# Optimization experiments

Measured on AMD Instinct MI355X. Metric: run time of the kernel, lower is better.

## Reference

```python
import jax, jax.numpy as jnp
import numpy as np

B, D, C = 4096, 2048, 64
L_HP, D_HP, OMEGA, EPSILON = 0.5, 1.0, 100.0, 0.1
LN_EPS = 1e-5
CLASS_COUNTS = [5000,4500,4050,3645,3280,2952,2657,2391,2152,1937,1743,1569,1412,1271,1144,1029,926,834,750,675,608,547,492,443,399,359,323,291,262,236,212,191,172,155,139,125,113,101,91,82,74,66,60,54,48,43,39,35,32,28,26,23,21,19,17,15,14,12,11,10,9,8,7,7]


def setup_inputs() -> dict:
    key = jax.random.key(0)
    k_x, k_y, k_b, k_u1, k_u2 = jax.random.split(key, 5)
    counts = jnp.asarray(CLASS_COUNTS, dtype=jnp.float32)
    # set_class_weights: tilde_C = 1/log(counts*d + eps), min-max normalized, scaled by l
    tilde = 1.0 / jnp.log(counts * D_HP + EPSILON)
    c = (tilde - jnp.min(tilde)) / (jnp.max(tilde) - jnp.min(tilde)) * L_HP
    # set_fs_classes: 1 where count <= omega
    fs_classes = jnp.where(counts <= OMEGA, 1, 0).astype(jnp.int32)
    x = jax.random.normal(k_x, (B, D), dtype=jnp.float32)
    y = jax.random.randint(k_y, (B,), 0, C)
    beta_idx = jax.random.randint(k_b, (B,), 0, B)
    u1 = jax.random.uniform(k_u1, (B,))
    u2 = jax.random.uniform(k_u2, (B,))
    alpha = jnp.where(u1 > 0.5, u2, jnp.ones((B,), jnp.float32))
    return {"x": x, "y": y, "alpha": alpha, "beta_idx": beta_idx, "c": c, "fs_classes": fs_classes}


def reference(x, y, alpha, beta_idx, c, fs_classes):
    n_batch, dim = x.shape
    num_classes = c.shape[0]
    # --- reconstruct ---
    mu = jnp.mean(x, axis=-1, keepdims=True)
    var = jnp.mean((x - mu) ** 2, axis=-1, keepdims=True)
    x_norm = (x - mu) / jnp.sqrt(var + LN_EPS) / jnp.sqrt(jnp.asarray(dim, x.dtype))
    sim = jnp.matmul(x_norm, x_norm.T)  # [B, B]
    # E[i, j] = eye[i, j] + fs_mask[j]  (broadcast over rows), thresholded to {0, 1}
    fs_mask = fs_classes[y].astype(x.dtype)  # [B]
    E = jnp.eye(n_batch, dtype=x.dtype) + fs_mask[None, :]
    E = jnp.where(E >= 1.0, 1.0, 0.0)
    sim = jax.nn.softmax(sim - 100000.0 * E, axis=-1)
    contrib = c[y]  # [B]
    reconstructions = jnp.matmul(sim, x)  # [B, D]
    R = reconstructions * contrib[:, None] + x * (1.0 - contrib)[:, None]
    # --- pairwise_mix: M @ R with M[i,:] = alpha[i]*e_i + (1-alpha[i])*e_{beta_idx[i]} ---
    y_oh = jax.nn.one_hot(y, num_classes, dtype=x.dtype)
    a = alpha[:, None]
    x_mix = a * R + (1.0 - a) * R[beta_idx]
    y_mix = a * y_oh + (1.0 - a) * y_oh[beta_idx]
    return (x_mix, y_mix)
```

## Files before the change

### kernel.cpp

```cpp
#include <hip/hip_runtime.h>
#include <cstdint>
#include <cstddef>

typedef __bf16 bf16;
typedef __bf16 bf16x8 __attribute__((ext_vector_type(8)));
typedef float floatx4 __attribute__((ext_vector_type(4)));
typedef int intx8 __attribute__((ext_vector_type(8)));

#define NB 4096
#define ND 2048
#define NCLS 64
#define TS 80
#define OS 72

__device__ __forceinline__ void stage16(const void* g, void* l) {
  __builtin_amdgcn_global_load_lds(
      (__attribute__((address_space(1))) unsigned int*)g,
      (__attribute__((address_space(3))) unsigned int*)l, 16, 0, 0);
}

__device__ __forceinline__ unsigned char fp8x1(float f) {
  return (unsigned char)(__builtin_amdgcn_cvt_pk_fp8_f32(f, f, 0, false) & 0xFF);
}
__device__ __forceinline__ int fp8x4(float f0, float f1, float f2, float f3) {
  int d = __builtin_amdgcn_cvt_pk_fp8_f32(f0, f1, 0, false);
  return __builtin_amdgcn_cvt_pk_fp8_f32(f2, f3, d, true);
}

__device__ __forceinline__ void gemm_core64(
    const unsigned char* __restrict__ Abase, const int aoff[4],
    const unsigned char* __restrict__ Bbase, const int boff[2], int nk,
    unsigned char* __restrict__ As0, unsigned char* __restrict__ Bs0,
    unsigned char* __restrict__ As1, unsigned char* __restrict__ Bs1,
    floatx4 acc[2][4], int w, int lane) {
  const int lm = lane & 15, quad = lane >> 4;
  auto STAGE = [&](int k0, unsigned char* As, unsigned char* Bs) {
#pragma unroll
    for (int q = 0; q < 4; ++q)
      stage16(Abase + (size_t)(aoff[q] + k0), As + w * 4096 + q * 1024);
#pragma unroll
    for (int q = 0; q < 2; ++q)
      stage16(Bbase + (size_t)(boff[q] + k0), Bs + w * 2048 + q * 1024);
  };
  STAGE(0, As0, Bs0);
  for (int k = 0; k < nk; ++k) {
    __syncthreads();
    if (k + 1 < nk)
      STAGE((k + 1) << 7, (k & 1) ? As0 : As1, (k & 1) ? Bs0 : Bs1);
    const unsigned char* Ac = (k & 1) ? As1 : As0;
    const unsigned char* Bc = (k & 1) ? Bs1 : Bs0;

    intx8 af[2], bf[4];
#pragma unroll
    for (int i = 0; i < 2; ++i) {
      const int row = w * 32 + i * 16 + lm;
      const int c0 = (quad * 2) ^ (row & 7);
      const int4 lo = *(const int4*)(Ac + row * 128 + c0 * 16);
      const int4 hi = *(const int4*)(Ac + row * 128 + (c0 ^ 1) * 16);
      af[i][0] = lo.x; af[i][1] = lo.y; af[i][2] = lo.z; af[i][3] = lo.w;
      af[i][4] = hi.x; af[i][5] = hi.y; af[i][6] = hi.z; af[i][7] = hi.w;
    }
#pragma unroll
    for (int i = 0; i < 4; ++i) {
      const int row = i * 16 + lm;
      const int c0 = (quad * 2) ^ (row & 7);
      const int4 lo = *(const int4*)(Bc + row * 128 + c0 * 16);
      const int4 hi = *(const int4*)(Bc + row * 128 + (c0 ^ 1) * 16);
      bf[i][0] = lo.x; bf[i][1] = lo.y; bf[i][2] = lo.z; bf[i][3] = lo.w;
      bf[i][4] = hi.x; bf[i][5] = hi.y; bf[i][6] = hi.z; bf[i][7] = hi.w;
    }
#pragma unroll
    for (int mi = 0; mi < 2; ++mi)
#pragma unroll
      for (int ni = 0; ni < 4; ++ni)
        acc[mi][ni] = __builtin_amdgcn_mfma_scale_f32_16x16x128_f8f6f4(
            af[mi], bf[ni], acc[mi][ni], 0, 0, 0, 127, 0, 127);
  }
}


__global__ __launch_bounds__(1024) void perm_kernel(
    const int* __restrict__ y, const int* __restrict__ fs,
    const float* __restrict__ c, int* __restrict__ perm,
    int* __restrict__ minfo, float* __restrict__ lrow,
    float* __restrict__ contrib) {
  const int t = threadIdx.x;
  const int base = t * 4;
  int fl[4];
  int cnt = 0;
#pragma unroll
  for (int j = 0; j < 4; ++j) {
    const int yi = y[base + j];
    fl[j] = (fs[yi] == 0) ? 1 : 0;
    cnt += fl[j];
    contrib[base + j] = c[yi];
    lrow[base + j] = 0.0f;
  }
  const int lane = t & 63, w = t >> 6;
  int inc = cnt;
#pragma unroll
  for (int o = 1; o < 64; o <<= 1) {
    int v = __shfl_up(inc, o);
    if (lane >= o) inc += v;
  }
  __shared__ int wsum[16];
  __shared__ int Msh;
  if (lane == 63) wsum[w] = inc;
  __syncthreads();
  int wbase = 0;
  for (int i = 0; i < w; ++i) wbase += wsum[i];
  int pos = wbase + inc - cnt;
#pragma unroll
  for (int j = 0; j < 4; ++j)
    if (fl[j]) perm[pos++] = base + j;
  if (t == 1023) Msh = wbase + inc;
  __syncthreads();
  const int M = Msh;
  const int Mp = (M + 127) & ~127;
  if (t < Mp - M) perm[M + t] = 0;
  if (t == 0) {
    minfo[0] = M;
    minfo[1] = Mp;
    minfo[2] = Mp >> 7;
  }
}

__global__ __launch_bounds__(256) void prep_kernel(
    const float* __restrict__ x, unsigned char* __restrict__ XN8,
    unsigned char* __restrict__ XBT8, const int* __restrict__ perm,
    const int* __restrict__ minfo) {
  __shared__ float tile[64][65];
  const int t = threadIdx.x;

  if (blockIdx.x < NB) {
    const int row = blockIdx.x;
    const float4* xr = (const float4*)(x + (size_t)row * ND);
    float4 v0 = xr[t], v1 = xr[t + 256];
    float s = v0.x + v0.y + v0.z + v0.w + v1.x + v1.y + v1.z + v1.w;
    float q = v0.x * v0.x + v0.y * v0.y + v0.z * v0.z + v0.w * v0.w +
              v1.x * v1.x + v1.y * v1.y + v1.z * v1.z + v1.w * v1.w;
#pragma unroll
    for (int o = 32; o > 0; o >>= 1) {
      s += __shfl_down(s, o);
      q += __shfl_down(q, o);
    }
    const int w = t >> 6;
    if ((t & 63) == 0) { tile[0][w] = s; tile[1][w] = q; }
    __syncthreads();
    s = tile[0][0] + tile[0][1] + tile[0][2] + tile[0][3];
    q = tile[1][0] + tile[1][1] + tile[1][2] + tile[1][3];
    const float mu = s * (1.0f / ND);
    const float var = q * (1.0f / ND) - mu * mu;
    const float sc =
        rsqrtf(var + 1e-5f) * 0.02209708691207961f * 32.0f;

    int* orow = (int*)(XN8 + (size_t)row * ND);
    orow[t] = fp8x4((v0.x - mu) * sc, (v0.y - mu) * sc, (v0.z - mu) * sc,
                    (v0.w - mu) * sc);
    orow[256 + t] = fp8x4((v1.x - mu) * sc, (v1.y - mu) * sc, (v1.z - mu) * sc,
                          (v1.w - mu) * sc);
  } else {
    const int b2 = blockIdx.x - NB;
    const int rb = b2 & 63;
    const int cb = b2 >> 6;
    if (rb * 64 >= minfo[1]) return;
    const int tx = t & 63, ty = t >> 6;
#pragma unroll
    for (int rr = ty; rr < 64; rr += 4)
      tile[rr][tx] = x[(size_t)perm[rb * 64 + rr] * ND + cb * 64 + tx];
    __syncthreads();
    const int ro = t >> 2;
    const int co = t & 3;
    int4 v;
    {
      const int j = co * 16;
      v.x = fp8x4(tile[j + 0][ro], tile[j + 1][ro], tile[j + 2][ro], tile[j + 3][ro]);
      v.y = fp8x4(tile[j + 4][ro], tile[j + 5][ro], tile[j + 6][ro], tile[j + 7][ro]);
      v.z = fp8x4(tile[j + 8][ro], tile[j + 9][ro], tile[j + 10][ro], tile[j + 11][ro]);
      v.w = fp8x4(tile[j + 12][ro], tile[j + 13][ro], tile[j + 14][ro], tile[j + 15][ro]);
    }
    *(int4*)(XBT8 + (size_t)(cb * 64 + ro) * NB + rb * 64 + co * 16) = v;
  }
}

__global__ __launch_bounds__(256, 3) void gemm_sim_kernel(
    const unsigned char* __restrict__ XN8, unsigned char* __restrict__ P8,
    float* __restrict__ lrow, const int* __restrict__ perm,
    const int* __restrict__ minfo) {
  __shared__ unsigned char smem[49152];
  unsigned char* As0 = smem;
  unsigned char* As1 = smem + 16384;
  unsigned char* Bs0 = smem + 32768;
  unsigned char* Bs1 = smem + 40960;

  const int Mp = minfo[1];
  const int id = blockIdx.x;
  const int xcd = id & 7;
  const int s = id >> 3;
  const int bi = xcd * 4 + (s & 3);
  const int bjc = s >> 2;
  const int n0 = bjc * 64;
  if (n0 >= Mp) return;
  const int M = minfo[0];
  const int m0 = bi * 128;

  const int t = threadIdx.x, w = t >> 6, lane = t & 63;
  const int lm = lane & 15, quad = lane >> 4;

  int aoff[4], boff[2];
#pragma unroll
  for (int q = 0; q < 4; ++q) {
    const int slot = w * 256 + q * 64 + lane;
    const int row = slot >> 3;
    const int cc = (slot & 7) ^ (row & 7);
    aoff[q] = (m0 + row) * ND + cc * 16;
  }
#pragma unroll
  for (int q = 0; q < 2; ++q) {
    const int slot = w * 128 + q * 64 + lane;
    const int row = slot >> 3;
    const int cc = (slot & 7) ^ (row & 7);
    boff[q] = perm[n0 + row] * ND + cc * 16;
  }

  floatx4 acc[2][4];
#pragma unroll
  for (int i = 0; i < 2; ++i)
#pragma unroll
    for (int j = 0; j < 4; ++j) acc[i][j] = 0.0f;

  gemm_core64(XN8, aoff, XN8, boff, ND >> 7, As0, Bs0, As1, Bs1, acc, w, lane);

  int pcol[4], valid[4];
#pragma unroll
  for (int ni = 0; ni < 4; ++ni) {
    const int gc = n0 + ni * 16 + lm;
    valid[ni] = (gc < M) ? 1 : 0;
    pcol[ni] = perm[gc];
  }

  float rs[2][4];
#pragma unroll
  for (int mi = 0; mi < 2; ++mi)
#pragma unroll
    for (int r = 0; r < 4; ++r) rs[mi][r] = 0.0f;

#pragma unroll
  for (int ni = 0; ni < 4; ++ni) {
#pragma unroll
    for (int mi = 0; mi < 2; ++mi) {
#pragma unroll
      for (int r = 0; r < 4; ++r) {
        const int grow = m0 + w * 32 + mi * 16 + quad * 4 + r;
        const float e = (valid[ni] && grow != pcol[ni])
                            ? __expf(acc[mi][ni][r] * 0.0009765625f)
                            : 0.0f;
        acc[mi][ni][r] = e;
        rs[mi][r] += e;
      }
    }
  }
#pragma unroll
  for (int mi = 0; mi < 2; ++mi)
#pragma unroll
    for (int r = 0; r < 4; ++r) {
      float vsum = rs[mi][r];
      vsum += __shfl_xor(vsum, 1);
      vsum += __shfl_xor(vsum, 2);
      vsum += __shfl_xor(vsum, 4);
      vsum += __shfl_xor(vsum, 8);
      if (lm == 0)
        atomicAdd(&lrow[m0 + w * 32 + mi * 16 + quad * 4 + r], vsum);
    }

  __syncthreads();
#pragma unroll
  for (int ni = 0; ni < 4; ++ni) {
    const int col = ni * 16 + lm;
#pragma unroll
    for (int mi = 0; mi < 2; ++mi)
#pragma unroll
      for (int r = 0; r < 4; ++r) {
        const int row = w * 32 + mi * 16 + quad * 4 + r;
        smem[row * TS + col] = fp8x1(acc[mi][ni][r]);
      }
  }
  __syncthreads();
#pragma unroll
  for (int it = 0; it < 2; ++it) {
    const int row = it * 64 + (t >> 2), ch = t & 3;
    int4 v = *(const int4*)(smem + row * TS + ch * 16);
    *(int4*)(P8 + (size_t)(m0 + row) * NB + n0 + ch * 16) = v;
  }
}

__global__ __launch_bounds__(256, 3) void gemm_recon_kernel(
    const unsigned char* __restrict__ P8, const unsigned char* __restrict__ XBT8,
    const float* __restrict__ x, const float* __restrict__ lrow,
    const float* __restrict__ contrib, const int* __restrict__ minfo,
    bf16* __restrict__ R) {
  __shared__ unsigned char smem[49152];
  unsigned char* As0 = smem;
  unsigned char* As1 = smem + 16384;
  unsigned char* Bs0 = smem + 32768;
  unsigned char* Bs1 = smem + 40960;

  const int id = blockIdx.x;
  const int xcd = id & 7;
  const int s = id >> 3;
  const int by = xcd * 4 + (s & 3);
  const int bx = s >> 2;
  const int m0 = by * 128, n0 = bx * 64;

  const int t = threadIdx.x, w = t >> 6, lane = t & 63;
  const int lm = lane & 15, quad = lane >> 4;

  int aoff[4], boff[2];
#pragma unroll
  for (int q = 0; q < 4; ++q) {
    const int slot = w * 256 + q * 64 + lane;
    const int row = slot >> 3;
    const int cc = (slot & 7) ^ (row & 7);
    aoff[q] = (m0 + row) * NB + cc * 16;
  }
#pragma unroll
  for (int q = 0; q < 2; ++q) {
    const int slot = w * 128 + q * 64 + lane;
    const int row = slot >> 3;
    const int cc = (slot & 7) ^ (row & 7);
    boff[q] = (n0 + row) * NB + cc * 16;
  }

  floatx4 acc[2][4];
#pragma unroll
  for (int i = 0; i < 2; ++i)
#pragma unroll
    for (int j = 0; j < 4; ++j) acc[i][j] = 0.0f;

  gemm_core64(P8, aoff, XBT8, boff, minfo[2], As0, Bs0, As1, Bs1, acc, w,
              lane);

  __syncthreads();
  bf16* osm = (bf16*)smem;
#pragma unroll
  for (int mi = 0; mi < 2; ++mi) {
#pragma unroll
    for (int r = 0; r < 4; ++r) {
      const int lrow_i = w * 32 + mi * 16 + quad * 4 + r;
      const int grow = m0 + lrow_i;
      const float inv = 1.0f / lrow[grow];
      const float ci = contrib[grow];
#pragma unroll
      for (int ni = 0; ni < 4; ++ni) {
        const int lcol = ni * 16 + lm;
        const float rec = acc[mi][ni][r] * inv;
        const float xv = x[(size_t)grow * ND + n0 + lcol];
        osm[lrow_i * OS + lcol] = (bf16)(rec * ci + xv * (1.0f - ci));
      }
    }
  }
  __syncthreads();
#pragma unroll
  for (int it = 0; it < 4; ++it) {
    const int row = it * 32 + (t >> 3), ch = t & 7;
    int4 v = *(const int4*)(osm + row * OS + ch * 8);
    *(int4*)(R + (size_t)(m0 + row) * ND + n0 + ch * 8) = v;
  }
}

__global__ __launch_bounds__(256) void mix_kernel(
    const bf16* __restrict__ R, const float* __restrict__ alpha,
    const int* __restrict__ beta_idx, const int* __restrict__ y,
    float* __restrict__ out) {
  const int t = threadIdx.x;
#pragma unroll
  for (int rr = 0; rr < 2; ++rr) {
    const int i = blockIdx.x * 2 + rr;
    const float a = alpha[i];
    const int bi = beta_idx[i];
    const bf16x8* Ri = (const bf16x8*)(R + (size_t)i * ND);
    const bf16x8* Rb = (const bf16x8*)(R + (size_t)bi * ND);
    const float b = 1.0f - a;
    bf16x8 r = Ri[t], g = Rb[t];
    float4 o0, o1;
    o0.x = a * (float)r[0] + b * (float)g[0];
    o0.y = a * (float)r[1] + b * (float)g[1];
    o0.z = a * (float)r[2] + b * (float)g[2];
    o0.w = a * (float)r[3] + b * (float)g[3];
    o1.x = a * (float)r[4] + b * (float)g[4];
    o1.y = a * (float)r[5] + b * (float)g[5];
    o1.z = a * (float)r[6] + b * (float)g[6];
    o1.w = a * (float)r[7] + b * (float)g[7];
    float4* o = (float4*)(out + (size_t)i * ND + t * 8);
    o[0] = o0;
    o[1] = o1;
    if (t < NCLS) {
      const int yi = y[i], yb = y[bi];
      const float v = a * (t == yi ? 1.0f : 0.0f) + b * (t == yb ? 1.0f : 0.0f);
      out[(size_t)NB * ND + (size_t)i * NCLS + t] = v;
    }
  }
}

extern "C" void kernel_launch(void* const* d_in, const int* in_sizes, int n_in,
                              void* d_out, int out_size, void* d_ws,
                              size_t ws_size, hipStream_t stream) {
  const float* x = (const float*)d_in[0];
  const int* y = (const int*)d_in[1];
  const float* alpha = (const float*)d_in[2];
  const int* beta = (const int*)d_in[3];
  const float* c = (const float*)d_in[4];
  const int* fs = (const int*)d_in[5];
  float* out = (float*)d_out;
  char* ws = (char*)d_ws;

  unsigned char* XN8  = (unsigned char*)(ws + 0);
  unsigned char* XBT8 = (unsigned char*)(ws + 8388608);
  unsigned char* P8   = (unsigned char*)(ws + 16777216);
  bf16* R   = (bf16*)(ws + 33554432);
  float* LR = (float*)(ws + 50331648);
  float* CT = (float*)(ws + 50331648 + 16384);
  int* PERM = (int*)(ws + 50331648 + 32768);
  int* MINFO = (int*)(ws + 50331648 + 49152);

  perm_kernel<<<1, 1024, 0, stream>>>(y, fs, c, PERM, MINFO, LR, CT);
  prep_kernel<<<NB + 2048, 256, 0, stream>>>(x, XN8, XBT8, PERM, MINFO);
  gemm_sim_kernel<<<1280, 256, 0, stream>>>(XN8, P8, LR, PERM, MINFO);
  gemm_recon_kernel<<<1024, 256, 0, stream>>>(P8, XBT8, x, LR, CT, MINFO, R);
  mix_kernel<<<NB / 2, 256, 0, stream>>>(R, alpha, beta, y, out);
}
```

Baseline: 169.6 us.

## Triple-buffer GEMM LDS staging with explicit vmcnt waits

Replaces the double-buffered LDS staging in the shared fp8 GEMM core with a three-stage ring buffer that prefetches two k-tiles ahead. Explicit s_waitcnt vmcnt waits and raw s_barrier replace __syncthreads, so loads for the next tile can stay in flight while the current one is consumed. LDS per block grows from 48KB to 72KB and launch bounds drop from 3 to 2 blocks per CU, trading occupancy for deeper prefetch.

```diff
diff --git a/kernel.cpp b/kernel.cpp
--- a/kernel.cpp
+++ b/kernel.cpp
@@ -30,52 +30,77 @@
 __device__ __forceinline__ void gemm_core64(
     const unsigned char* __restrict__ Abase, const int aoff[4],
     const unsigned char* __restrict__ Bbase, const int boff[2], int nk,
-    unsigned char* __restrict__ As0, unsigned char* __restrict__ Bs0,
-    unsigned char* __restrict__ As1, unsigned char* __restrict__ Bs1,
-    floatx4 acc[2][4], int w, int lane) {
+    unsigned char* __restrict__ smem, floatx4 acc[2][4], int w, int lane) {
   const int lm = lane & 15, quad = lane >> 4;
-  auto STAGE = [&](int k0, unsigned char* As, unsigned char* Bs) {
-#pragma unroll
-    for (int q = 0; q < 4; ++q)
-      stage16(Abase + (size_t)(aoff[q] + k0), As + w * 4096 + q * 1024);
-#pragma unroll
-    for (int q = 0; q < 2; ++q)
-      stage16(Bbase + (size_t)(boff[q] + k0), Bs + w * 2048 + q * 1024);
-  };
-  STAGE(0, As0, Bs0);
-  for (int k = 0; k < nk; ++k) {
-    __syncthreads();
-    if (k + 1 < nk)
-      STAGE((k + 1) << 7, (k & 1) ? As0 : As1, (k & 1) ? Bs0 : Bs1);
-    const unsigned char* Ac = (k & 1) ? As1 : As0;
-    const unsigned char* Bc = (k & 1) ? Bs1 : Bs0;
-
-    intx8 af[2], bf[4];
-#pragma unroll
-    for (int i = 0; i < 2; ++i) {
-      const int row = w * 32 + i * 16 + lm;
-      const int c0 = (quad * 2) ^ (row & 7);
-      const int4 lo = *(const int4*)(Ac + row * 128 + c0 * 16);
-      const int4 hi = *(const int4*)(Ac + row * 128 + (c0 ^ 1) * 16);
-      af[i][0] = lo.x; af[i][1] = lo.y; af[i][2] = lo.z; af[i][3] = lo.w;
-      af[i][4] = hi.x; af[i][5] = hi.y; af[i][6] = hi.z; af[i][7] = hi.w;
-    }
-#pragma unroll
-    for (int i = 0; i < 4; ++i) {
-      const int row = i * 16 + lm;
-      const int c0 = (quad * 2) ^ (row & 7);
-      const int4 lo = *(const int4*)(Bc + row * 128 + c0 * 16);
-      const int4 hi = *(const int4*)(Bc + row * 128 + (c0 ^ 1) * 16);
-      bf[i][0] = lo.x; bf[i][1] = lo.y; bf[i][2] = lo.z; bf[i][3] = lo.w;
-      bf[i][4] = hi.x; bf[i][5] = hi.y; bf[i][6] = hi.z; bf[i][7] = hi.w;
-    }
-#pragma unroll
-    for (int mi = 0; mi < 2; ++mi)
-#pragma unroll
-      for (int ni = 0; ni < 4; ++ni)
-        acc[mi][ni] = __builtin_amdgcn_mfma_scale_f32_16x16x128_f8f6f4(
-            af[mi], bf[ni], acc[mi][ni], 0, 0, 0, 127, 0, 127);
-  }
+  unsigned char* b0 = smem;
+  unsigned char* b1 = smem + 24576;
+  unsigned char* b2 = smem + 49152;
+
+#define STG_(k0, buf)                                                      \
+  do {                                                                     \
+    stage16(Abase + (size_t)(aoff[0] + (k0)), (buf) + w * 4096);           \
+    stage16(Abase + (size_t)(aoff[1] + (k0)), (buf) + w * 4096 + 1024);    \
+    stage16(Abase + (size_t)(aoff[2] + (k0)), (buf) + w * 4096 + 2048);    \
+    stage16(Abase + (size_t)(aoff[3] + (k0)), (buf) + w * 4096 + 3072);    \
+    stage16(Bbase + (size_t)(boff[0] + (k0)), (buf) + 16384 + w * 2048);   \
+    stage16(Bbase + (size_t)(boff[1] + (k0)),                              \
+            (buf) + 16384 + w * 2048 + 1024);                              \
+  } while (0)
+
+  STG_(0, b0);
+  __builtin_amdgcn_sched_barrier(0);
+  if (1 < nk) STG_(128, b1);
+
+#define STEP3_(kk, cur, nxt2)                                             \
+  do {                                                                    \
+    if ((kk) + 1 < nk)                                                    \
+      asm volatile("s_waitcnt vmcnt(6) lgkmcnt(0)" ::: "memory");         \
+    else                                                                  \
+      asm volatile("s_waitcnt vmcnt(0) lgkmcnt(0)" ::: "memory");         \
+    __builtin_amdgcn_s_barrier();                                         \
+    if ((kk) + 2 < nk) STG_(((kk) + 2) << 7, nxt2);                       \
+    const unsigned char* Ac = (cur);                                      \
+    const unsigned char* Bc = (cur) + 16384;                              \
+    intx8 af[2], bf[4];                                                   \
+    _Pragma("unroll")                                                     \
+    for (int i = 0; i < 2; ++i) {                                         \
+      const int row = w * 32 + i * 16 + lm;                               \
+      const int c0 = (quad * 2) ^ (row & 7);                              \
+      const int4 lo = *(const int4*)(Ac + row * 128 + c0 * 16);           \
+      const int4 hi = *(const int4*)(Ac + row * 128 + (c0 ^ 1) * 16);     \
+      af[i][0] = lo.x; af[i][1] = lo.y; af[i][2] = lo.z;                  \
+      af[i][3] = lo.w; af[i][4] = hi.x; af[i][5] = hi.y;                  \
+      af[i][6] = hi.z; af[i][7] = hi.w;                                   \
+    }                                                                     \
+    _Pragma("unroll")                                                     \
+    for (int i = 0; i < 4; ++i) {                                         \
+      const int row = i * 16 + lm;                                        \
+      const int c0 = (quad * 2) ^ (row & 7);                              \
+      const int4 lo = *(const int4*)(Bc + row * 128 + c0 * 16);           \
+      const int4 hi = *(const int4*)(Bc + row * 128 + (c0 ^ 1) * 16);     \
+      bf[i][0] = lo.x; bf[i][1] = lo.y; bf[i][2] = lo.z;                  \
+      bf[i][3] = lo.w; bf[i][4] = hi.x; bf[i][5] = hi.y;                  \
+      bf[i][6] = hi.z; bf[i][7] = hi.w;                                   \
+    }                                                                     \
+    _Pragma("unroll")                                                     \
+    for (int mi = 0; mi < 2; ++mi)                                        \
+      _Pragma("unroll")                                                   \
+      for (int ni = 0; ni < 4; ++ni)                                      \
+        acc[mi][ni] = __builtin_amdgcn_mfma_scale_f32_16x16x128_f8f6f4(   \
+            af[mi], bf[ni], acc[mi][ni], 0, 0, 0, 127, 0, 127);           \
+  } while (0)
+
+  int k = 0;
+  while (true) {
+    STEP3_(k, b0, b2);
+    if (++k >= nk) break;
+    STEP3_(k, b1, b0);
+    if (++k >= nk) break;
+    STEP3_(k, b2, b1);
+    if (++k >= nk) break;
+  }
+#undef STEP3_
+#undef STG_
 }
 
 
@@ -183,15 +208,11 @@
   }
 }
 
-__global__ __launch_bounds__(256, 3) void gemm_sim_kernel(
+__global__ __launch_bounds__(256, 2) void gemm_sim_kernel(
     const unsigned char* __restrict__ XN8, unsigned char* __restrict__ P8,
     float* __restrict__ lrow, const int* __restrict__ perm,
     const int* __restrict__ minfo) {
-  __shared__ unsigned char smem[49152];
-  unsigned char* As0 = smem;
-  unsigned char* As1 = smem + 16384;
-  unsigned char* Bs0 = smem + 32768;
-  unsigned char* Bs1 = smem + 40960;
+  __shared__ unsigned char smem[73728];
 
   const int Mp = minfo[1];
   const int id = blockIdx.x;
@@ -229,7 +250,7 @@
 #pragma unroll
     for (int j = 0; j < 4; ++j) acc[i][j] = 0.0f;
 
-  gemm_core64(XN8, aoff, XN8, boff, ND >> 7, As0, Bs0, As1, Bs1, acc, w, lane);
+  gemm_core64(XN8, aoff, XN8, boff, ND >> 7, smem, acc, w, lane);
 
   int pcol[4], valid[4];
 #pragma unroll
@@ -294,16 +315,12 @@
   }
 }
 
-__global__ __launch_bounds__(256, 3) void gemm_recon_kernel(
+__global__ __launch_bounds__(256, 2) void gemm_recon_kernel(
     const unsigned char* __restrict__ P8, const unsigned char* __restrict__ XBT8,
     const float* __restrict__ x, const float* __restrict__ lrow,
     const float* __restrict__ contrib, const int* __restrict__ minfo,
     bf16* __restrict__ R) {
-  __shared__ unsigned char smem[49152];
-  unsigned char* As0 = smem;
-  unsigned char* As1 = smem + 16384;
-  unsigned char* Bs0 = smem + 32768;
-  unsigned char* Bs1 = smem + 40960;
+  __shared__ unsigned char smem[73728];
 
   const int id = blockIdx.x;
   const int xcd = id & 7;
@@ -337,8 +354,7 @@
 #pragma unroll
     for (int j = 0; j < 4; ++j) acc[i][j] = 0.0f;
 
-  gemm_core64(P8, aoff, XBT8, boff, minfo[2], As0, Bs0, As1, Bs1, acc, w,
-              lane);
+  gemm_core64(P8, aoff, XBT8, boff, minfo[2], smem, acc, w, lane);
 
   __syncthreads();
   bf16* osm = (bf16*)smem;
```

Measured after the change: 170.8 us. No clear change (+0.7%).

## Merge perm into row-norm kernel and transpose-cast into sim GEMM launch

Applied to the files above, without the earlier changes.

The standalone permutation kernel becomes block 0 of a new prep kernel that also does the per-row LayerNorm and fp8 quantization. The transposed fp8 copy of the permuted x moves out of that kernel and into extra blocks appended to the similarity GEMM grid, since the GEMM does not depend on it. This cuts one kernel launch and lets the transpose work overlap the GEMM tiles. In exchange, the GEMM grid becomes heterogeneous, and the transpose blocks compete with GEMM blocks for CU slots and LDS.

```diff
diff --git a/kernel.cpp b/kernel.cpp
--- a/kernel.cpp
+++ b/kernel.cpp
@@ -12,6 +12,7 @@
 #define NCLS 64
 #define TS 80
 #define OS 72
+#define SIMGRID 1280
 
 __device__ __forceinline__ void stage16(const void* g, void* l) {
   __builtin_amdgcn_global_load_lds(
@@ -79,91 +80,101 @@
 }
 
 
-__global__ __launch_bounds__(1024) void perm_kernel(
-    const int* __restrict__ y, const int* __restrict__ fs,
-    const float* __restrict__ c, int* __restrict__ perm,
+__global__ __launch_bounds__(256) void prep1_kernel(
+    const float* __restrict__ x, const int* __restrict__ y,
+    const int* __restrict__ fs, const float* __restrict__ c,
+    unsigned char* __restrict__ XN8, int* __restrict__ perm,
     int* __restrict__ minfo, float* __restrict__ lrow,
     float* __restrict__ contrib) {
   const int t = threadIdx.x;
-  const int base = t * 4;
-  int fl[4];
-  int cnt = 0;
-#pragma unroll
-  for (int j = 0; j < 4; ++j) {
-    const int yi = y[base + j];
-    fl[j] = (fs[yi] == 0) ? 1 : 0;
-    cnt += fl[j];
-    contrib[base + j] = c[yi];
-    lrow[base + j] = 0.0f;
-  }
-  const int lane = t & 63, w = t >> 6;
-  int inc = cnt;
-#pragma unroll
-  for (int o = 1; o < 64; o <<= 1) {
-    int v = __shfl_up(inc, o);
-    if (lane >= o) inc += v;
-  }
-  __shared__ int wsum[16];
+  __shared__ float red[2][4];
+  __shared__ int wsum[4];
   __shared__ int Msh;
-  if (lane == 63) wsum[w] = inc;
+
+  if (blockIdx.x == 0) {
+    const int base = t * 16;
+    unsigned fl = 0;
+    int cnt = 0;
+#pragma unroll
+    for (int j = 0; j < 16; ++j) {
+      const int yi = y[base + j];
+      const unsigned u = (fs[yi] == 0) ? 1u : 0u;
+      fl |= u << j;
+      cnt += (int)u;
+      contrib[base + j] = c[yi];
+      lrow[base + j] = 0.0f;
+    }
+    const int lane = t & 63, w = t >> 6;
+    int inc = cnt;
+#pragma unroll
+    for (int o = 1; o < 64; o <<= 1) {
+      int v = __shfl_up(inc, o);
+      if (lane >= o) inc += v;
+    }
+    if (lane == 63) wsum[w] = inc;
+    __syncthreads();
+    int wbase = 0;
+    for (int i = 0; i < w; ++i) wbase += wsum[i];
+    int pos = wbase + inc - cnt;
+#pragma unroll
+    for (int j = 0; j < 16; ++j)
+      if ((fl >> j) & 1u) perm[pos++] = base + j;
+    if (t == 255) Msh = wbase + inc;
+    __syncthreads();
+    const int M = Msh;
+    const int Mp = (M + 127) & ~127;
+    if (t < Mp - M) perm[M + t] = 0;
+    if (t == 0) {
+      minfo[0] = M;
+      minfo[1] = Mp;
+      minfo[2] = Mp >> 7;
+    }
+    return;
+  }
+
+  const int row = blockIdx.x - 1;
+  const float4* xr = (const float4*)(x + (size_t)row * ND);
+  float4 v0 = xr[t], v1 = xr[t + 256];
+  float s = v0.x + v0.y + v0.z + v0.w + v1.x + v1.y + v1.z + v1.w;
+  float q = v0.x * v0.x + v0.y * v0.y + v0.z * v0.z + v0.w * v0.w +
+            v1.x * v1.x + v1.y * v1.y + v1.z * v1.z + v1.w * v1.w;
+#pragma unroll
+  for (int o = 32; o > 0; o >>= 1) {
+    s += __shfl_down(s, o);
+    q += __shfl_down(q, o);
+  }
+  const int w = t >> 6;
+  if ((t & 63) == 0) { red[0][w] = s; red[1][w] = q; }
   __syncthreads();
-  int wbase = 0;
-  for (int i = 0; i < w; ++i) wbase += wsum[i];
-  int pos = wbase + inc - cnt;
-#pragma unroll
-  for (int j = 0; j < 4; ++j)
-    if (fl[j]) perm[pos++] = base + j;
-  if (t == 1023) Msh = wbase + inc;
-  __syncthreads();
-  const int M = Msh;
-  const int Mp = (M + 127) & ~127;
-  if (t < Mp - M) perm[M + t] = 0;
-  if (t == 0) {
-    minfo[0] = M;
-    minfo[1] = Mp;
-    minfo[2] = Mp >> 7;
-  }
-}
-
-__global__ __launch_bounds__(256) void prep_kernel(
-    const float* __restrict__ x, unsigned char* __restrict__ XN8,
-    unsigned char* __restrict__ XBT8, const int* __restrict__ perm,
+  s = red[0][0] + red[0][1] + red[0][2] + red[0][3];
+  q = red[1][0] + red[1][1] + red[1][2] + red[1][3];
+  const float mu = s * (1.0f / ND);
+  const float var = q * (1.0f / ND) - mu * mu;
+  const float sc =
+      rsqrtf(var + 1e-5f) * 0.02209708691207961f * 32.0f;
+
+  int* orow = (int*)(XN8 + (size_t)row * ND);
+  orow[t] = fp8x4((v0.x - mu) * sc, (v0.y - mu) * sc, (v0.z - mu) * sc,
+                  (v0.w - mu) * sc);
+  orow[256 + t] = fp8x4((v1.x - mu) * sc, (v1.y - mu) * sc, (v1.z - mu) * sc,
+                        (v1.w - mu) * sc);
+}
+
+__global__ __launch_bounds__(256, 3) void gemm_sim_kernel(
+    const unsigned char* __restrict__ XN8, const float* __restrict__ x,
+    unsigned char* __restrict__ P8, unsigned char* __restrict__ XBT8,
+    float* __restrict__ lrow, const int* __restrict__ perm,
     const int* __restrict__ minfo) {
-  __shared__ float tile[64][65];
+  __shared__ unsigned char smem[49152];
+  const int Mp = minfo[1];
   const int t = threadIdx.x;
 
-  if (blockIdx.x < NB) {
-    const int row = blockIdx.x;
-    const float4* xr = (const float4*)(x + (size_t)row * ND);
-    float4 v0 = xr[t], v1 = xr[t + 256];
-    float s = v0.x + v0.y + v0.z + v0.w + v1.x + v1.y + v1.z + v1.w;
-    float q = v0.x * v0.x + v0.y * v0.y + v0.z * v0.z + v0.w * v0.w +
-              v1.x * v1.x + v1.y * v1.y + v1.z * v1.z + v1.w * v1.w;
-#pragma unroll
-    for (int o = 32; o > 0; o >>= 1) {
-      s += __shfl_down(s, o);
-      q += __shfl_down(q, o);
-    }
-    const int w = t >> 6;
-    if ((t & 63) == 0) { tile[0][w] = s; tile[1][w] = q; }
-    __syncthreads();
-    s = tile[0][0] + tile[0][1] + tile[0][2] + tile[0][3];
-    q = tile[1][0] + tile[1][1] + tile[1][2] + tile[1][3];
-    const float mu = s * (1.0f / ND);
-    const float var = q * (1.0f / ND) - mu * mu;
-    const float sc =
-        rsqrtf(var + 1e-5f) * 0.02209708691207961f * 32.0f;
-
-    int* orow = (int*)(XN8 + (size_t)row * ND);
-    orow[t] = fp8x4((v0.x - mu) * sc, (v0.y - mu) * sc, (v0.z - mu) * sc,
-                    (v0.w - mu) * sc);
-    orow[256 + t] = fp8x4((v1.x - mu) * sc, (v1.y - mu) * sc, (v1.z - mu) * sc,
-                          (v1.w - mu) * sc);
-  } else {
-    const int b2 = blockIdx.x - NB;
+  if (blockIdx.x >= SIMGRID) {
+    const int b2 = blockIdx.x - SIMGRID;
     const int rb = b2 & 63;
     const int cb = b2 >> 6;
-    if (rb * 64 >= minfo[1]) return;
+    if (rb * 64 >= Mp) return;
+    float(*tile)[65] = (float(*)[65])smem;
     const int tx = t & 63, ty = t >> 6;
 #pragma unroll
     for (int rr = ty; rr < 64; rr += 4)
@@ -180,20 +191,14 @@
       v.w = fp8x4(tile[j + 12][ro], tile[j + 13][ro], tile[j + 14][ro], tile[j + 15][ro]);
     }
     *(int4*)(XBT8 + (size_t)(cb * 64 + ro) * NB + rb * 64 + co * 16) = v;
-  }
-}
-
-__global__ __launch_bounds__(256, 3) void gemm_sim_kernel(
-    const unsigned char* __restrict__ XN8, unsigned char* __restrict__ P8,
-    float* __restrict__ lrow, const int* __restrict__ perm,
-    const int* __restrict__ minfo) {
-  __shared__ unsigned char smem[49152];
+    return;
+  }
+
   unsigned char* As0 = smem;
   unsigned char* As1 = smem + 16384;
   unsigned char* Bs0 = smem + 32768;
   unsigned char* Bs1 = smem + 40960;
 
-  const int Mp = minfo[1];
   const int id = blockIdx.x;
   const int xcd = id & 7;
   const int s = id >> 3;
@@ -204,7 +209,7 @@
   const int M = minfo[0];
   const int m0 = bi * 128;
 
-  const int t = threadIdx.x, w = t >> 6, lane = t & 63;
+  const int w = t >> 6, lane = t & 63;
   const int lm = lane & 15, quad = lane >> 4;
 
   int aoff[4], boff[2];
@@ -423,9 +428,10 @@
   int* PERM = (int*)(ws + 50331648 + 32768);
   int* MINFO = (int*)(ws + 50331648 + 49152);
 
-  perm_kernel<<<1, 1024, 0, stream>>>(y, fs, c, PERM, MINFO, LR, CT);
-  prep_kernel<<<NB + 2048, 256, 0, stream>>>(x, XN8, XBT8, PERM, MINFO);
-  gemm_sim_kernel<<<1280, 256, 0, stream>>>(XN8, P8, LR, PERM, MINFO);
+  prep1_kernel<<<NB + 1, 256, 0, stream>>>(x, y, fs, c, XN8, PERM, MINFO, LR,
+                                           CT);
+  gemm_sim_kernel<<<SIMGRID + 2048, 256, 0, stream>>>(XN8, x, P8, XBT8, LR,
+                                                      PERM, MINFO);
   gemm_recon_kernel<<<1024, 256, 0, stream>>>(P8, XBT8, x, LR, CT, MINFO, R);
   mix_kernel<<<NB / 2, 256, 0, stream>>>(R, alpha, beta, y, out);
 }
```

New measurement: 170.3 us. No clear change (+0.4%).
